# Optimization experiments

Measured on AMD Instinct MI355X. Metric: run time of the kernel, lower is better.

## Reference

```python
import jax, jax.numpy as jnp
import numpy as np
import math

NUM_HEADS = 16
SEQ_LEN = 2048
K_OFFSET = 37
P = 2


def get_slopes(n):
    def pow2(m):
        start = 2 ** (-2 ** (-(math.log2(m) - 3)))
        return [start * start ** i for i in range(m)]
    if math.log2(n).is_integer():
        return pow2(n)
    c = 2 ** math.floor(math.log2(n))
    return pow2(c) + get_slopes(2 * c)[0::2][: n - c]


def setup_inputs() -> dict:
    key = jax.random.key(0)
    k1, k2, k3 = jax.random.split(key, 3)
    x = jax.random.normal(k1, (2, 2048, 1024), jnp.float32)  # only dtype is used
    # delta ~ Gamma(concentration=2, rate=1), shape (P, d) with d=1
    delta = jax.random.gamma(k2, 2.0, (P, 1)).astype(jnp.float32)
    # u ~ Uniform(0, delta)
    u = jax.random.uniform(k3, (P, 1), jnp.float32) * delta
    return {"x": x, "delta": delta, "u": u, "seq_len": SEQ_LEN, "k": K_OFFSET}


def reference(x, delta, u, seq_len, k):
    dtype = x.dtype
    N = seq_len
    # positions t = arange(k, seq_len + k), shape (N, 1) == rbf input X
    t = jnp.arange(k, seq_len + k, dtype=dtype).reshape(-1, 1)

    def one_binning(delta_p, u_p):
        # ceil-binning; since t is strictly increasing, bin ids are nondecreasing,
        # so torch.unique's inverse_indices == cumulative rank of bin changes.
        idx = jnp.ceil((t - u_p) / delta_p).astype(jnp.int32)       # (N, 1)
        change = jnp.any(idx[1:] != idx[:-1], axis=-1).astype(jnp.int32)  # (N-1,)
        inv = jnp.concatenate([jnp.zeros((1,), jnp.int32), jnp.cumsum(change)])  # (N,)
        # one-hot over unique bins, padded to N columns (extra columns are zero)
        return (inv[:, None] == jnp.arange(N, dtype=jnp.int32)[None, :]).astype(dtype)

    Zp = jax.vmap(one_binning)(delta, u)                 # (P, N, N)
    Pn = Zp.shape[0]
    Z = jnp.transpose(Zp, (1, 0, 2)).reshape(N, Pn * N)  # hstack over P
    Z = Z / jnp.sqrt(jnp.asarray(Pn, dtype))

    slopes = jnp.asarray(get_slopes(NUM_HEADS), dtype)
    sqrt_slopes = jnp.sqrt(jnp.exp(slopes)).reshape(NUM_HEADS, 1, 1)
    alibi = (sqrt_slopes * Z[None, :, :])[None]          # (1, H, N, P*N)
    return jnp.transpose(alibi, (2, 0, 1, 3))            # (N, 1, H, P*N)
```

## Files before the change

### kernel.cpp

```cpp
#include <hip/hip_runtime.h>
#include <hip/hip_bf16.h>


#define N_SEQ 2048
#define H_NUM 16
#define P_NUM 2

__device__ __forceinline__ int bin_idx(int kk, int m, float up, float dp) {
    return (int)ceilf(((float)(kk + m) - up) / dp);
}

__global__ __launch_bounds__(256) void scan_scatter_kernel(
        const float* __restrict__ delta, const float* __restrict__ u,
        const int* __restrict__ kptr, float* __restrict__ out) {
    const int blk = blockIdx.x;
    const int tid = threadIdx.x;
    const int n0  = blk << 3;
    const int kk  = kptr[0];

    __shared__ int s_cnt[P_NUM];
    __shared__ int s_wpre[P_NUM][8];

    if (tid < P_NUM) s_cnt[tid] = 0;
    if (tid < P_NUM) {
        const int p = tid;
        const float dp = delta[p], up = u[p];
        int acc = 0;
        s_wpre[p][0] = 0;
        int prev = bin_idx(kk, n0, up, dp);
        for (int d = 1; d < 8; ++d) {
            int cur = bin_idx(kk, n0 + d, up, dp);
            acc += (cur != prev) ? 1 : 0;
            prev = cur;
            s_wpre[p][d] = acc;
        }
    }
    __syncthreads();

    {
        const int p = tid >> 7;
        const float dp = delta[p], up = u[p];
        int local = 0;
        for (int m = 1 + (tid & 127); m <= n0; m += 128) {
            int a = bin_idx(kk, m,     up, dp);
            int b = bin_idx(kk, m - 1, up, dp);
            local += (a != b) ? 1 : 0;
        }
        #pragma unroll
        for (int off = 32; off > 0; off >>= 1)
            local += __shfl_down(local, off, 64);
        if ((tid & 63) == 0) atomicAdd(&s_cnt[p], local);
    }
    __syncthreads();

    const int dn = tid >> 5;
    const int h  = (tid >> 1) & 15;
    const int p  = tid & 1;
    const int n  = n0 + dn;
    const int col = s_cnt[p] + s_wpre[p][dn];

    const float slope = exp2f(-0.5f * (float)(h + 1));
    const float val = sqrtf(expf(slope)) * 0.70710678118f;

    out[(size_t)((n << 4) + h) * 4096u + (size_t)(p << 11) + (size_t)col] = val;
}

extern "C" void kernel_launch(void* const* d_in, const int* in_sizes, int n_in,
                              void* d_out, int out_size, void* d_ws, size_t ws_size,
                              hipStream_t stream) {
    const float* delta = (const float*)d_in[1];
    const float* u     = (const float*)d_in[2];
    const int*   kptr  = (const int*)d_in[4];

    hipMemsetAsync(d_out, 0, (size_t)out_size * sizeof(float), stream);

    scan_scatter_kernel<<<256, 256, 0, stream>>>(delta, u, kptr, (float*)d_out);
}
```

Measured before the change: 100.5 us.

## Fuse zero-fill and scatter into one kernel writing full rows with vector stores

Removes the separate memset pass and the scattered single-element writes. A single kernel now writes every output element, zeros and the one-hot value alike, using 16-byte nontemporal stores, one block per sequence position. This cuts one full pass over the output and one extra launch. In exchange, each block recomputes the prefix scan of bin changes up to its own position, which is redundant work across blocks.

```diff
diff --git a/kernel.cpp b/kernel.cpp
--- a/kernel.cpp
+++ b/kernel.cpp
@@ -6,34 +6,26 @@
 #define H_NUM 16
 #define P_NUM 2
 
+typedef float fx4 __attribute__((ext_vector_type(4)));
+
 __device__ __forceinline__ int bin_idx(int kk, int m, float up, float dp) {
     return (int)ceilf(((float)(kk + m) - up) / dp);
 }
 
-__global__ __launch_bounds__(256) void scan_scatter_kernel(
+__global__ __launch_bounds__(256) void fused_fill_kernel(
         const float* __restrict__ delta, const float* __restrict__ u,
-        const int* __restrict__ kptr, float* __restrict__ out) {
-    const int blk = blockIdx.x;
+        const int* __restrict__ kptr, fx4* __restrict__ out) {
+    const int n   = blockIdx.x;
     const int tid = threadIdx.x;
-    const int n0  = blk << 3;
     const int kk  = kptr[0];
 
-    __shared__ int s_cnt[P_NUM];
-    __shared__ int s_wpre[P_NUM][8];
+    __shared__ int   s_cnt[P_NUM];
+    __shared__ float sval[H_NUM];
 
     if (tid < P_NUM) s_cnt[tid] = 0;
-    if (tid < P_NUM) {
-        const int p = tid;
-        const float dp = delta[p], up = u[p];
-        int acc = 0;
-        s_wpre[p][0] = 0;
-        int prev = bin_idx(kk, n0, up, dp);
-        for (int d = 1; d < 8; ++d) {
-            int cur = bin_idx(kk, n0 + d, up, dp);
-            acc += (cur != prev) ? 1 : 0;
-            prev = cur;
-            s_wpre[p][d] = acc;
-        }
+    if (tid < H_NUM) {
+        const float slope = exp2f(-0.5f * (float)(tid + 1));
+        sval[tid] = sqrtf(expf(slope)) * 0.70710678118f;
     }
     __syncthreads();
 
@@ -41,7 +33,7 @@
         const int p = tid >> 7;
         const float dp = delta[p], up = u[p];
         int local = 0;
-        for (int m = 1 + (tid & 127); m <= n0; m += 128) {
+        for (int m = 1 + (tid & 127); m <= n; m += 128) {
             int a = bin_idx(kk, m,     up, dp);
             int b = bin_idx(kk, m - 1, up, dp);
             local += (a != b) ? 1 : 0;
@@ -53,16 +45,27 @@
     }
     __syncthreads();
 
-    const int dn = tid >> 5;
-    const int h  = (tid >> 1) & 15;
-    const int p  = tid & 1;
-    const int n  = n0 + dn;
-    const int col = s_cnt[p] + s_wpre[p][dn];
+    const int inv0 = s_cnt[0];
+    const int inv1 = s_cnt[1];
 
-    const float slope = exp2f(-0.5f * (float)(h + 1));
-    const float val = sqrtf(expf(slope)) * 0.70710678118f;
+    fx4* __restrict__ slab = out + (size_t)n * 16384u;
 
-    out[(size_t)((n << 4) + h) * 4096u + (size_t)(p << 11) + (size_t)col] = val;
+    #pragma unroll 4
+    for (int j = 0; j < 64; ++j) {
+        const int pos  = tid + (j << 8);
+        const int h    = pos >> 10;
+        const float v  = sval[h];
+        const int col0 = (pos & 1023) << 2;
+        const int tgt  = (col0 & 2048) ? inv1 : inv0;
+        const int c    = col0 & 2047;
+
+        fx4 o;
+        o.x = (tgt == c)     ? v : 0.0f;
+        o.y = (tgt == c + 1) ? v : 0.0f;
+        o.z = (tgt == c + 2) ? v : 0.0f;
+        o.w = (tgt == c + 3) ? v : 0.0f;
+        __builtin_nontemporal_store(o, &slab[pos]);
+    }
 }
 
 extern "C" void kernel_launch(void* const* d_in, const int* in_sizes, int n_in,
@@ -72,7 +75,5 @@
     const float* u     = (const float*)d_in[2];
     const int*   kptr  = (const int*)d_in[4];
 
-    hipMemsetAsync(d_out, 0, (size_t)out_size * sizeof(float), stream);
-
-    scan_scatter_kernel<<<256, 256, 0, stream>>>(delta, u, kptr, (float*)d_out);
+    fused_fill_kernel<<<N_SEQ, 256, 0, stream>>>(delta, u, kptr, (fx4*)d_out);
 }
```

After: 101.8 us. No clear change (+1.3%).
